# Kernel tuning notes

Hardware: AMD Instinct MI355X
Metric: run time of the kernel (lower is better)

## Reference

```python
import jax, jax.numpy as jnp
import numpy as np

N = 4096
IN_F = 512
OUT_F = 256
HEADS = 4
HEAD_DIM = OUT_F // HEADS


def setup_inputs() -> dict:
    key = jax.random.key(0)
    k_feat, k_adj, k_w, k_a = jax.random.split(key, 4)
    features = jax.random.normal(k_feat, (N, IN_F), dtype=jnp.float32)
    adj_matrix = jax.random.uniform(k_adj, (N, N), dtype=jnp.float32)
    # xavier-uniform-ish init scaled small
    W = jax.random.normal(k_w, (OUT_F, IN_F), dtype=jnp.float32) * (1.0 / np.sqrt(IN_F))
    a = jax.random.normal(k_a, (HEADS, 2 * HEAD_DIM), dtype=jnp.float32) * 0.1
    bias = jnp.zeros((OUT_F,), dtype=jnp.float32)
    return {"features": features, "adj_matrix": adj_matrix, "W": W, "a": a, "bias": bias}


def reference(features, adj_matrix, W, a, bias):
    n = features.shape[0]
    h = features @ W.T                      # [N, OUT_F]
    hh = h.reshape(n, HEADS, HEAD_DIM)      # [N, H, D]
    # e[i,j,h] = leaky_relu(<h_i, a[:, :D]> + <h_j, a[:, D:]>) -- additive decomposition
    e_src = jnp.einsum('nhd,hd->nh', hh, a[:, :HEAD_DIM])   # [N, H]
    e_dst = jnp.einsum('nhd,hd->nh', hh, a[:, HEAD_DIM:])   # [N, H]
    e = e_src[:, None, :] + e_dst[None, :, :]               # [N, N, H]
    e = jnp.where(e >= 0, e, 0.2 * e)                       # leaky_relu(0.2)
    mask = adj_matrix[:, :, None] > 0.1                     # [N, N, 1]
    e = jnp.where(mask, e, -jnp.inf)
    attention = jax.nn.softmax(e, axis=1)                   # softmax over j
    attention = jnp.nan_to_num(attention, nan=0.0)          # fully-masked rows -> 0
    attention_mean = attention.mean(axis=2)                 # [N, N]
    h_out = attention_mean @ h + bias                       # [N, OUT_F]
    return h_out
```

## Files before the change

### kernel.cpp

```cpp
#include <hip/hip_runtime.h>
#include <math.h>

#define NN      4096
#define INF_    512
#define OUTF    256
#define NHEAD   4
#define HDIM    64
#define KSPLIT  8

typedef __attribute__((ext_vector_type(8))) short  short8x;
typedef __attribute__((ext_vector_type(4))) float  float4x;

__device__ __forceinline__ unsigned short f2bf(float x) {
    union { float f; unsigned int u; } c; c.f = x;
    unsigned int r = (c.u + 0x7FFFu + ((c.u >> 16) & 1u)) >> 16;
    return (unsigned short)r;
}
__device__ __forceinline__ float bflo(unsigned int u) {
    union { unsigned int x; float f; } c; c.x = u << 16; return c.f;
}
__device__ __forceinline__ float bfhi(unsigned int u) {
    union { unsigned int x; float f; } c; c.x = u & 0xFFFF0000u; return c.f;
}

__global__ __launch_bounds__(256) void k_cast(const float* __restrict__ feat,
                                              const float* __restrict__ W,
                                              unsigned short* __restrict__ featb,
                                              unsigned short* __restrict__ Wb) {
    const int b = blockIdx.x;
    const float* src;
    unsigned short* dst;
    int idx;
    if (b < 2048) { src = feat; dst = featb; idx = b * 1024 + threadIdx.x * 4; }
    else          { src = W;    dst = Wb;    idx = (b - 2048) * 1024 + threadIdx.x * 4; }
    float4x v = *(const float4x*)(src + idx);
    ushort4 u;
    u.x = f2bf(v[0]); u.y = f2bf(v[1]); u.z = f2bf(v[2]); u.w = f2bf(v[3]);
    *(ushort4*)(dst + idx) = u;
}

__global__ __launch_bounds__(256) void k_hedge(const unsigned short* __restrict__ featb,
                                               const unsigned short* __restrict__ Wb,
                                               const float* __restrict__ a,
                                               unsigned short* __restrict__ hT,
                                               float* __restrict__ es,
                                               unsigned short* __restrict__ Bt,
                                               unsigned short* __restrict__ Dt) {
    __shared__ __align__(16) unsigned short lds_f[64 * 40];
    __shared__ __align__(16) unsigned short lds_w[256 * 40];
    const int tid  = threadIdx.x;
    const int w    = tid >> 6;
    const int lane = tid & 63;
    const int lidx = lane & 15;
    const int quad = lane >> 4;
    const int i0   = blockIdx.x * 64;
    const int sr = tid >> 2;
    const int skq = (tid & 3) * 8;

    float4x acc[4][4];
    #pragma unroll
    for (int p = 0; p < 4; ++p)
        #pragma unroll
        for (int q = 0; q < 4; ++q)
            acc[p][q] = (float4x){0.f, 0.f, 0.f, 0.f};

    for (int kt = 0; kt < INF_; kt += 32) {
        __syncthreads();
        *(ushort4*)&lds_f[sr * 40 + skq]     = *(const ushort4*)&featb[(size_t)(i0 + sr) * INF_ + kt + skq];
        *(ushort4*)&lds_f[sr * 40 + skq + 4] = *(const ushort4*)&featb[(size_t)(i0 + sr) * INF_ + kt + skq + 4];
        #pragma unroll
        for (int itr = 0; itr < 4; ++itr) {
            int n = itr * 64 + sr;
            *(ushort4*)&lds_w[n * 40 + skq]     = *(const ushort4*)&Wb[(size_t)n * INF_ + kt + skq];
            *(ushort4*)&lds_w[n * 40 + skq + 4] = *(const ushort4*)&Wb[(size_t)n * INF_ + kt + skq + 4];
        }
        __syncthreads();
        short8x af[4], bw[4];
        #pragma unroll
        for (int t = 0; t < 4; ++t) {
            af[t] = *(const short8x*)&lds_f[(t * 16 + lidx) * 40 + quad * 8];
            bw[t] = *(const short8x*)&lds_w[(w * 64 + t * 16 + lidx) * 40 + quad * 8];
        }
        #pragma unroll
        for (int it = 0; it < 4; ++it)
            #pragma unroll
            for (int nt = 0; nt < 4; ++nt)
                acc[it][nt] = __builtin_amdgcn_mfma_f32_16x16x32_bf16(
                    af[it], bw[nt], acc[it][nt], 0, 0, 0);
    }
    #pragma unroll
    for (int it = 0; it < 4; ++it)
        #pragma unroll
        for (int nt = 0; nt < 4; ++nt) {
            int col = w * 64 + nt * 16 + lidx;
            int m0r = i0 + it * 16 + quad * 4;
            ushort4 u;
            u.x = f2bf(acc[it][nt][0]); u.y = f2bf(acc[it][nt][1]);
            u.z = f2bf(acc[it][nt][2]); u.w = f2bf(acc[it][nt][3]);
            *(ushort4*)&hT[(size_t)col * NN + m0r] = u;
        }
    float asrc[4], adst[4];
    #pragma unroll
    for (int nt = 0; nt < 4; ++nt) {
        asrc[nt] = a[w * 2 * HDIM + nt * 16 + lidx];
        adst[nt] = a[w * 2 * HDIM + HDIM + nt * 16 + lidx];
    }
    #pragma unroll
    for (int it = 0; it < 4; ++it)
        #pragma unroll
        for (int r = 0; r < 4; ++r) {
            float s = 0.f, d = 0.f;
            #pragma unroll
            for (int nt = 0; nt < 4; ++nt) {
                s += acc[it][nt][r] * asrc[nt];
                d += acc[it][nt][r] * adst[nt];
            }
            #pragma unroll
            for (int off = 1; off < 16; off <<= 1) {
                s += __shfl_xor(s, off);
                d += __shfl_xor(d, off);
            }
            if (lidx == 0) {
                int row = i0 + it * 16 + quad * 4 + r;
                es[row * NHEAD + w] = s;
                Bt[row * NHEAD + w] = f2bf(__expf(d));
                Dt[row * NHEAD + w] = f2bf(__expf(0.2f * d));
            }
        }
}

__global__ __launch_bounds__(256) void k_attn(const float* __restrict__ adj,
                                              const float* __restrict__ es,
                                              const unsigned short* __restrict__ Bt,
                                              const unsigned short* __restrict__ Dt,
                                              unsigned short* __restrict__ attn) {
    __shared__ float red[4][8];
    __shared__ float cfs[8];
    const int tid = threadIdx.x;
    const int wv  = tid >> 6;
    const int lane = tid & 63;
    const int i = blockIdx.x;

    const float4x esv = ((const float4x*)es)[i];
    float TB[4];
    #pragma unroll
    for (int h = 0; h < 4; ++h) TB[h] = __expf(-esv[h]);
    const float4x* arow4 = (const float4x*)(adj + (size_t)i * NN);
    const uint4* B4 = (const uint4*)Bt;
    const uint4* D4 = (const uint4*)Dt;

    float4x av[4];
    float S1[4] = {0.f, 0.f, 0.f, 0.f};
    float S2[4] = {0.f, 0.f, 0.f, 0.f};
    #pragma unroll
    for (int t = 0; t < 4; ++t) {
        int jv = t * 256 + tid;
        av[t] = arow4[jv];
        uint4 bu0 = B4[jv * 2], bu1 = B4[jv * 2 + 1];
        uint4 du0 = D4[jv * 2], du1 = D4[jv * 2 + 1];
        unsigned int bwv[8] = {bu0.x, bu0.y, bu0.z, bu0.w, bu1.x, bu1.y, bu1.z, bu1.w};
        unsigned int dwv[8] = {du0.x, du0.y, du0.z, du0.w, du1.x, du1.y, du1.z, du1.w};
        #pragma unroll
        for (int u = 0; u < 4; ++u) {
            bool m = av[t][u] > 0.1f;
            float b0 = bflo(bwv[u * 2]), b1 = bfhi(bwv[u * 2]);
            float b2 = bflo(bwv[u * 2 + 1]), b3 = bfhi(bwv[u * 2 + 1]);
            float d0 = bflo(dwv[u * 2]), d1 = bfhi(dwv[u * 2]);
            float d2 = bflo(dwv[u * 2 + 1]), d3 = bfhi(dwv[u * 2 + 1]);
            bool p0 = b0 >= TB[0], p1 = b1 >= TB[1], p2 = b2 >= TB[2], p3 = b3 >= TB[3];
            S1[0] += (m && p0) ? b0 : 0.f;   S2[0] += (m && !p0) ? d0 : 0.f;
            S1[1] += (m && p1) ? b1 : 0.f;   S2[1] += (m && !p1) ? d1 : 0.f;
            S1[2] += (m && p2) ? b2 : 0.f;   S2[2] += (m && !p2) ? d2 : 0.f;
            S1[3] += (m && p3) ? b3 : 0.f;   S2[3] += (m && !p3) ? d3 : 0.f;
        }
    }
    #pragma unroll
    for (int off = 1; off < 64; off <<= 1) {
        #pragma unroll
        for (int h = 0; h < 4; ++h) {
            S1[h] += __shfl_xor(S1[h], off);
            S2[h] += __shfl_xor(S2[h], off);
        }
    }
    if (lane == 0) {
        #pragma unroll
        for (int h = 0; h < 4; ++h) { red[wv][h] = S1[h]; red[wv][4 + h] = S2[h]; }
    }
    __syncthreads();
    if (tid < 8)
        cfs[tid] = red[0][tid] + red[1][tid] + red[2][tid] + red[3][tid];
    __syncthreads();
    float cA[4], cC[4];
    #pragma unroll
    for (int h = 0; h < 4; ++h) {
        float A = __expf(esv[h]), C = __expf(0.2f * esv[h]);
        float den = A * cfs[h] + C * cfs[4 + h];
        float sc = den > 0.f ? 0.25f / den : 0.f;
        cA[h] = A * sc;
        cC[h] = C * sc;
    }

    unsigned short* orow = attn + (size_t)i * NN;
    #pragma unroll
    for (int t = 0; t < 4; ++t) {
        int jv = t * 256 + tid;
        uint4 bu0 = B4[jv * 2], bu1 = B4[jv * 2 + 1];
        uint4 du0 = D4[jv * 2], du1 = D4[jv * 2 + 1];
        unsigned int bwv[8] = {bu0.x, bu0.y, bu0.z, bu0.w, bu1.x, bu1.y, bu1.z, bu1.w};
        unsigned int dwv[8] = {du0.x, du0.y, du0.z, du0.w, du1.x, du1.y, du1.z, du1.w};
        ushort4 o;
        unsigned short* op = (unsigned short*)&o;
        #pragma unroll
        for (int u = 0; u < 4; ++u) {
            float b0 = bflo(bwv[u * 2]), b1 = bfhi(bwv[u * 2]);
            float b2 = bflo(bwv[u * 2 + 1]), b3 = bfhi(bwv[u * 2 + 1]);
            float d0 = bflo(dwv[u * 2]), d1 = bfhi(dwv[u * 2]);
            float d2 = bflo(dwv[u * 2 + 1]), d3 = bfhi(dwv[u * 2 + 1]);
            float p;
            p  = (b0 >= TB[0]) ? cA[0] * b0 : cC[0] * d0;
            p += (b1 >= TB[1]) ? cA[1] * b1 : cC[1] * d1;
            p += (b2 >= TB[2]) ? cA[2] * b2 : cC[2] * d2;
            p += (b3 >= TB[3]) ? cA[3] * b3 : cC[3] * d3;
            op[u] = f2bf((av[t][u] > 0.1f) ? p : 0.f);
        }
        *(ushort4*)&orow[jv * 4] = o;
    }
}

__global__ __launch_bounds__(256) void k_out_gemm(const unsigned short* __restrict__ attn,
                                                  const unsigned short* __restrict__ hT,
                                                  float* __restrict__ partials) {
    __shared__ __align__(16) unsigned short lds_a[64 * 40];
    __shared__ __align__(16) unsigned short lds_h[256 * 40];
    const int tid  = threadIdx.x;
    const int w    = tid >> 6;
    const int lane = tid & 63;
    const int lidx = lane & 15;
    const int quad = lane >> 4;
    const int i0    = blockIdx.x * 64;
    const int kbase = blockIdx.y * (NN / KSPLIT);
    const int srow = tid >> 3;
    const int skq  = tid & 7;

    float4x acc[4][4];
    #pragma unroll
    for (int p = 0; p < 4; ++p)
        #pragma unroll
        for (int q = 0; q < 4; ++q)
            acc[p][q] = (float4x){0.f, 0.f, 0.f, 0.f};

    ushort4 pa[2], ph[8];
    #pragma unroll
    for (int it = 0; it < 2; ++it)
        pa[it] = *(const ushort4*)&attn[(size_t)(i0 + it * 32 + srow) * NN + kbase + skq * 4];
    #pragma unroll
    for (int it = 0; it < 8; ++it)
        ph[it] = *(const ushort4*)&hT[(size_t)(it * 32 + srow) * NN + kbase + skq * 4];

    const int KSTEPS = (NN / KSPLIT) / 32;
    for (int ks = 0; ks < KSTEPS; ++ks) {
        __syncthreads();
        #pragma unroll
        for (int it = 0; it < 2; ++it)
            *(ushort4*)&lds_a[(it * 32 + srow) * 40 + skq * 4] = pa[it];
        #pragma unroll
        for (int it = 0; it < 8; ++it)
            *(ushort4*)&lds_h[(it * 32 + srow) * 40 + skq * 4] = ph[it];
        __syncthreads();
        if (ks < KSTEPS - 1) {
            const int ktn = kbase + (ks + 1) * 32;
            #pragma unroll
            for (int it = 0; it < 2; ++it)
                pa[it] = *(const ushort4*)&attn[(size_t)(i0 + it * 32 + srow) * NN + ktn + skq * 4];
            #pragma unroll
            for (int it = 0; it < 8; ++it)
                ph[it] = *(const ushort4*)&hT[(size_t)(it * 32 + srow) * NN + ktn + skq * 4];
        }
        short8x af[4], bfr[4];
        #pragma unroll
        for (int t = 0; t < 4; ++t) {
            af[t]  = *(const short8x*)&lds_a[(t * 16 + lidx) * 40 + quad * 8];
            bfr[t] = *(const short8x*)&lds_h[(w * 64 + t * 16 + lidx) * 40 + quad * 8];
        }
        #pragma unroll
        for (int it = 0; it < 4; ++it)
            #pragma unroll
            for (int nt = 0; nt < 4; ++nt)
                acc[it][nt] = __builtin_amdgcn_mfma_f32_16x16x32_bf16(
                    af[it], bfr[nt], acc[it][nt], 0, 0, 0);
    }
    float* pbase = partials + (size_t)blockIdx.y * NN * OUTF;
    #pragma unroll
    for (int it = 0; it < 4; ++it)
        #pragma unroll
        for (int nt = 0; nt < 4; ++nt)
            #pragma unroll
            for (int rr = 0; rr < 4; ++rr) {
                int row = i0 + it * 16 + quad * 4 + rr;
                int col = w * 64 + nt * 16 + lidx;
                pbase[(size_t)row * OUTF + col] = acc[it][nt][rr];
            }
}

__global__ __launch_bounds__(256) void k_reduce_out(const float* __restrict__ partials,
                                                    const float* __restrict__ bias,
                                                    float* __restrict__ out) {
    const int i = blockIdx.x;
    const int n = threadIdx.x;
    float acc = bias[n];
    #pragma unroll
    for (int s = 0; s < KSPLIT; ++s)
        acc += partials[((size_t)s * NN + i) * OUTF + n];
    out[(size_t)i * OUTF + n] = acc;
}

extern "C" void kernel_launch(void* const* d_in, const int* in_sizes, int n_in,
                              void* d_out, int out_size, void* d_ws, size_t ws_size,
                              hipStream_t stream) {
    const float* feat = (const float*)d_in[0];
    const float* adj  = (const float*)d_in[1];
    const float* W    = (const float*)d_in[2];
    const float* a    = (const float*)d_in[3];
    const float* bias = (const float*)d_in[4];
    float* out = (float*)d_out;

    char* ws = (char*)d_ws;
    float*          es    = (float*)(ws + 0);
    unsigned short* Btb   = (unsigned short*)(ws + (64u << 10));
    unsigned short* Dtb   = (unsigned short*)(ws + (96u << 10));
    unsigned short* hT    = (unsigned short*)(ws + (256u << 10));
    unsigned short* attn  = (unsigned short*)(ws + (2560u << 10));
    unsigned short* featb = (unsigned short*)(ws + (2560u << 10));
    unsigned short* Wb    = (unsigned short*)(ws + (6656u << 10));
    float*          partials = (float*)(ws + (35328u << 10));

    k_cast      <<<2176,             256, 0, stream>>>(feat, W, featb, Wb);
    k_hedge     <<<64,               256, 0, stream>>>(featb, Wb, a, hT, es, Btb, Dtb);
    k_attn      <<<NN,               256, 0, stream>>>(adj, es, Btb, Dtb, attn);
    k_out_gemm  <<<dim3(64, KSPLIT), 256, 0, stream>>>(attn, hT, partials);
    k_reduce_out<<<NN,               256, 0, stream>>>(partials, bias, out);
}
```

Baseline: 183.8 us.

## Shrink projection tiles to 16 rows, prefetch into registers, double output K-split

```diff
diff --git a/kernel.cpp b/kernel.cpp
--- a/kernel.cpp
+++ b/kernel.cpp
@@ -6,7 +6,7 @@
 #define OUTF    256
 #define NHEAD   4
 #define HDIM    64
-#define KSPLIT  8
+#define KSPLIT  16
 
 typedef __attribute__((ext_vector_type(8))) short  short8x;
 typedef __attribute__((ext_vector_type(4))) float  float4x;
@@ -46,59 +46,65 @@
                                                float* __restrict__ es,
                                                unsigned short* __restrict__ Bt,
                                                unsigned short* __restrict__ Dt) {
-    __shared__ __align__(16) unsigned short lds_f[64 * 40];
+    __shared__ __align__(16) unsigned short lds_f[16 * 40];
     __shared__ __align__(16) unsigned short lds_w[256 * 40];
     const int tid  = threadIdx.x;
     const int w    = tid >> 6;
     const int lane = tid & 63;
     const int lidx = lane & 15;
     const int quad = lane >> 4;
-    const int i0   = blockIdx.x * 64;
-    const int sr = tid >> 2;
-    const int skq = (tid & 3) * 8;
-
-    float4x acc[4][4];
-    #pragma unroll
-    for (int p = 0; p < 4; ++p)
-        #pragma unroll
-        for (int q = 0; q < 4; ++q)
-            acc[p][q] = (float4x){0.f, 0.f, 0.f, 0.f};
+    const int i0   = blockIdx.x * 16;
+    const int fr = (tid & 127) >> 3;
+    const int fk = (tid & 7) * 4;
+    const int wr = tid >> 3;
+    const int wk = (tid & 7) * 4;
+
+    float4x acc[4];
+    #pragma unroll
+    for (int nt = 0; nt < 4; ++nt) acc[nt] = (float4x){0.f, 0.f, 0.f, 0.f};
+
+    ushort4 pf{0,0,0,0};
+    ushort4 pw[8];
+    if (tid < 128)
+        pf = *(const ushort4*)&featb[(size_t)(i0 + fr) * INF_ + fk];
+    #pragma unroll
+    for (int it = 0; it < 8; ++it)
+        pw[it] = *(const ushort4*)&Wb[(size_t)(it * 32 + wr) * INF_ + wk];
 
     for (int kt = 0; kt < INF_; kt += 32) {
         __syncthreads();
-        *(ushort4*)&lds_f[sr * 40 + skq]     = *(const ushort4*)&featb[(size_t)(i0 + sr) * INF_ + kt + skq];
-        *(ushort4*)&lds_f[sr * 40 + skq + 4] = *(const ushort4*)&featb[(size_t)(i0 + sr) * INF_ + kt + skq + 4];
-        #pragma unroll
-        for (int itr = 0; itr < 4; ++itr) {
-            int n = itr * 64 + sr;
-            *(ushort4*)&lds_w[n * 40 + skq]     = *(const ushort4*)&Wb[(size_t)n * INF_ + kt + skq];
-            *(ushort4*)&lds_w[n * 40 + skq + 4] = *(const ushort4*)&Wb[(size_t)n * INF_ + kt + skq + 4];
-        }
+        if (tid < 128)
+            *(ushort4*)&lds_f[fr * 40 + fk] = pf;
+        #pragma unroll
+        for (int it = 0; it < 8; ++it)
+            *(ushort4*)&lds_w[(it * 32 + wr) * 40 + wk] = pw[it];
         __syncthreads();
-        short8x af[4], bw[4];
-        #pragma unroll
-        for (int t = 0; t < 4; ++t) {
-            af[t] = *(const short8x*)&lds_f[(t * 16 + lidx) * 40 + quad * 8];
-            bw[t] = *(const short8x*)&lds_w[(w * 64 + t * 16 + lidx) * 40 + quad * 8];
-        }
-        #pragma unroll
-        for (int it = 0; it < 4; ++it)
-            #pragma unroll
-            for (int nt = 0; nt < 4; ++nt)
-                acc[it][nt] = __builtin_amdgcn_mfma_f32_16x16x32_bf16(
-                    af[it], bw[nt], acc[it][nt], 0, 0, 0);
-    }
-    #pragma unroll
-    for (int it = 0; it < 4; ++it)
-        #pragma unroll
-        for (int nt = 0; nt < 4; ++nt) {
-            int col = w * 64 + nt * 16 + lidx;
-            int m0r = i0 + it * 16 + quad * 4;
-            ushort4 u;
-            u.x = f2bf(acc[it][nt][0]); u.y = f2bf(acc[it][nt][1]);
-            u.z = f2bf(acc[it][nt][2]); u.w = f2bf(acc[it][nt][3]);
-            *(ushort4*)&hT[(size_t)col * NN + m0r] = u;
-        }
+        if (kt + 32 < INF_) {
+            const int kn = kt + 32;
+            if (tid < 128)
+                pf = *(const ushort4*)&featb[(size_t)(i0 + fr) * INF_ + kn + fk];
+            #pragma unroll
+            for (int it = 0; it < 8; ++it)
+                pw[it] = *(const ushort4*)&Wb[(size_t)(it * 32 + wr) * INF_ + kn + wk];
+        }
+        short8x af = *(const short8x*)&lds_f[lidx * 40 + quad * 8];
+        short8x bw[4];
+        #pragma unroll
+        for (int nt = 0; nt < 4; ++nt)
+            bw[nt] = *(const short8x*)&lds_w[(w * 64 + nt * 16 + lidx) * 40 + quad * 8];
+        #pragma unroll
+        for (int nt = 0; nt < 4; ++nt)
+            acc[nt] = __builtin_amdgcn_mfma_f32_16x16x32_bf16(af, bw[nt], acc[nt], 0, 0, 0);
+    }
+    #pragma unroll
+    for (int nt = 0; nt < 4; ++nt) {
+        int col = w * 64 + nt * 16 + lidx;
+        int m0r = i0 + quad * 4;
+        ushort4 u;
+        u.x = f2bf(acc[nt][0]); u.y = f2bf(acc[nt][1]);
+        u.z = f2bf(acc[nt][2]); u.w = f2bf(acc[nt][3]);
+        *(ushort4*)&hT[(size_t)col * NN + m0r] = u;
+    }
     float asrc[4], adst[4];
     #pragma unroll
     for (int nt = 0; nt < 4; ++nt) {
@@ -106,27 +112,25 @@
         adst[nt] = a[w * 2 * HDIM + HDIM + nt * 16 + lidx];
     }
     #pragma unroll
-    for (int it = 0; it < 4; ++it)
-        #pragma unroll
-        for (int r = 0; r < 4; ++r) {
-            float s = 0.f, d = 0.f;
-            #pragma unroll
-            for (int nt = 0; nt < 4; ++nt) {
-                s += acc[it][nt][r] * asrc[nt];
-                d += acc[it][nt][r] * adst[nt];
-            }
-            #pragma unroll
-            for (int off = 1; off < 16; off <<= 1) {
-                s += __shfl_xor(s, off);
-                d += __shfl_xor(d, off);
-            }
-            if (lidx == 0) {
-                int row = i0 + it * 16 + quad * 4 + r;
-                es[row * NHEAD + w] = s;
-                Bt[row * NHEAD + w] = f2bf(__expf(d));
-                Dt[row * NHEAD + w] = f2bf(__expf(0.2f * d));
-            }
-        }
+    for (int r = 0; r < 4; ++r) {
+        float s = 0.f, d = 0.f;
+        #pragma unroll
+        for (int nt = 0; nt < 4; ++nt) {
+            s += acc[nt][r] * asrc[nt];
+            d += acc[nt][r] * adst[nt];
+        }
+        #pragma unroll
+        for (int off = 1; off < 16; off <<= 1) {
+            s += __shfl_xor(s, off);
+            d += __shfl_xor(d, off);
+        }
+        if (lidx == 0) {
+            int row = i0 + quad * 4 + r;
+            es[row * NHEAD + w] = s;
+            Bt[row * NHEAD + w] = f2bf(__expf(d));
+            Dt[row * NHEAD + w] = f2bf(__expf(0.2f * d));
+        }
+    }
 }
 
 __global__ __launch_bounds__(256) void k_attn(const float* __restrict__ adj,
@@ -332,10 +336,10 @@
     unsigned short* attn  = (unsigned short*)(ws + (2560u << 10));
     unsigned short* featb = (unsigned short*)(ws + (2560u << 10));
     unsigned short* Wb    = (unsigned short*)(ws + (6656u << 10));
-    float*          partials = (float*)(ws + (35328u << 10));
+    float*          partials = (float*)(ws + (36864u << 10));
 
     k_cast      <<<2176,             256, 0, stream>>>(feat, W, featb, Wb);
-    k_hedge     <<<64,               256, 0, stream>>>(featb, Wb, a, hT, es, Btb, Dtb);
+    k_hedge     <<<256,              256, 0, stream>>>(featb, Wb, a, hT, es, Btb, Dtb);
     k_attn      <<<NN,               256, 0, stream>>>(adj, es, Btb, Dtb, attn);
     k_out_gemm  <<<dim3(64, KSPLIT), 256, 0, stream>>>(attn, hT, partials);
     k_reduce_out<<<NN,               256, 0, stream>>>(partials, bias, out);
```

Result: no change. 184.8 us (+0.5%).
